# Optimization experiments

Measured on AMD Instinct MI355X. Metric: run time of the kernel, lower is better.

The kernel has to match this reference:

```python
import jax, jax.numpy as jnp
import numpy as np


def setup_inputs() -> dict:
    key = jax.random.key(0)
    k1, k2, k3 = jax.random.split(key, 3)
    B, S, D, N = 2, 2048, 1024, 16
    H = D // N  # head_dim = 64
    x = jax.random.normal(k1, (B, S, D), dtype=jnp.float32)
    W_qkv = jax.random.normal(k2, (N, D, 3 * H), dtype=jnp.float32) / np.sqrt(D).astype(np.float32)
    W_out = jax.random.normal(k3, (N, H, D), dtype=jnp.float32) / np.sqrt(D).astype(np.float32)
    return {"x": x, "W_qkv": W_qkv, "W_out": W_out}


def reference(x, W_qkv, W_out):
    B, S, D = x.shape
    head_dim = W_qkv.shape[-1] // 3
    # QKV projection per head: [B, N, S, 3*H]
    qkv = jnp.einsum('bsd,ndh->bnsh', x, W_qkv)
    q, k, v = jnp.split(qkv, 3, axis=-1)  # each [B, N, S, H]
    scale = jnp.asarray(1.0 / np.sqrt(head_dim), dtype=x.dtype)
    attn = jnp.einsum('bnqh,bnkh->bnqk', q, k) * scale  # [B, N, S, S]
    # causal mask: -1e10 above the diagonal (matches buffer in original)
    mask = jnp.asarray(-1e10, dtype=x.dtype) * (1.0 - jnp.tril(jnp.ones((S, S), dtype=x.dtype)))
    attn = jax.nn.softmax(attn + mask, axis=-1)
    out = jnp.einsum('bnqk,bnkh->bnqh', attn, v)  # [B, N, S, H]
    # faithful to original: raw row-major reshape [B,N,S,H] -> [B, N*H, S]
    out = out.reshape(B, -1, S)
    # faithful to original einsum: d kept, n and h summed over W_out
    return jnp.einsum('bds,nhd->bsd', out, W_out)
```

## Files before the change

kernel.cpp:

```cpp
#include <hip/hip_runtime.h>
#include <hip/hip_bf16.h>

#define B_ 2
#define S_ 2048
#define D_ 1024
#define N_ 16
#define H_ 64

typedef unsigned short u16;
typedef unsigned int u32;
typedef __bf16 bf16x8 __attribute__((ext_vector_type(8)));
typedef u16 u16x8 __attribute__((ext_vector_type(8)));
typedef u32 u32x2 __attribute__((ext_vector_type(2)));
typedef float f4v __attribute__((ext_vector_type(4)));

__device__ __forceinline__ u16 f2b(float f) {
    u32 u = __builtin_bit_cast(u32, f);
    u32 r = (u + 0x7FFFu + ((u >> 16) & 1u)) >> 16;
    return (u16)r;
}
__device__ __forceinline__ bf16x8 asbf(u16x8 v) { return __builtin_bit_cast(bf16x8, v); }
__device__ __forceinline__ u32 cvtpk(float a, float b) {
    u32 r;
    asm("v_cvt_pk_bf16_f32 %0, %1, %2" : "=v"(r) : "v"(a), "v"(b));
    return r;
}

__global__ __launch_bounds__(256) void k_cvt_x(const float* __restrict__ x,
                                               u16* __restrict__ xb) {
    size_t i = ((size_t)blockIdx.x * 256 + threadIdx.x) * 8;
    float4 f0 = *(const float4*)(x + i);
    float4 f1 = *(const float4*)(x + i + 4);
    u16x8 o;
    o[0] = f2b(f0.x); o[1] = f2b(f0.y); o[2] = f2b(f0.z); o[3] = f2b(f0.w);
    o[4] = f2b(f1.x); o[5] = f2b(f1.y); o[6] = f2b(f1.z); o[7] = f2b(f1.w);
    *(u16x8*)(xb + i) = o;
}

__global__ __launch_bounds__(256) void k_cvt_w(const float* __restrict__ w,
                                               u16* __restrict__ wt) {
    __shared__ float T[64][65];
    const int d0 = blockIdx.x * 64, jt = blockIdx.y, n = blockIdx.z;
    const int j0 = jt * 64;
    const float sc = (jt == 0) ? 0.125f : 1.0f;
    const int t = threadIdx.x;
#pragma unroll
    for (int rep = 0; rep < 4; ++rep) {
        int v = t + rep * 256;
        int row = v >> 4, c4 = v & 15;
        float4 f = *(const float4*)(w + ((size_t)(n * 1024 + d0 + row)) * 192 + j0 + c4 * 4);
        T[row][c4 * 4 + 0] = f.x * sc;
        T[row][c4 * 4 + 1] = f.y * sc;
        T[row][c4 * 4 + 2] = f.z * sc;
        T[row][c4 * 4 + 3] = f.w * sc;
    }
    __syncthreads();
#pragma unroll
    for (int rep = 0; rep < 2; ++rep) {
        int c = t + rep * 256;
        int j = c >> 3, db = c & 7;
        u16x8 o;
#pragma unroll
        for (int e = 0; e < 8; ++e) o[e] = f2b(T[db * 8 + e][j]);
        *(u16x8*)(wt + ((size_t)(n * 192 + j0 + j)) * 1024 + d0 + db * 8) = o;
    }
}

__global__ __launch_bounds__(256) void k_wsum(const float* __restrict__ Wout,
                                              float* __restrict__ wsum) {
    __shared__ float red[16][17];
    const int dd = threadIdx.x & 15, rr = threadIdx.x >> 4;
    const int d = blockIdx.x * 16 + dd;
    float s = 0.f;
    for (int r = rr * 64; r < rr * 64 + 64; ++r) s += Wout[(size_t)r * 1024 + d];
    red[rr][dd] = s;
    __syncthreads();
    if (rr == 0) {
        float t = 0.f;
#pragma unroll
        for (int k = 0; k < 16; ++k) t += red[k][dd];
        wsum[d] = t;
    }
}

__global__ __launch_bounds__(512) void k_qkv(const u16* __restrict__ xb,
                                             const u16* __restrict__ wt,
                                             u16* __restrict__ qbuf,
                                             u16* __restrict__ kbuf,
                                             u16* __restrict__ vt) {
    __shared__ u16 As[128 * 64];
    __shared__ u16 Bst[192 * 64];
    const int st = blockIdx.x, n = blockIdx.y;
    const int t = threadIdx.x;
    const int w = t >> 6, lane = t & 63, hi2 = lane >> 4, lo4 = lane & 15;

    const int arow = t >> 2, aq4 = t & 3, ar7 = arow & 7;
    const u16* Ag = xb + (size_t)(st * 128 + arow) * 1024 + aq4 * 16;
    u16* Al0 = As + arow * 64 + ((aq4 * 16 + 0) ^ (ar7 << 3));
    u16* Al1 = As + arow * 64 + ((aq4 * 16 + 8) ^ (ar7 << 3));
    const int br0 = t >> 3, boff = t & 7;
    const u16* Bg0 = wt + (size_t)(n * 192 + br0) * 1024 + boff * 8;
    const u16* Bg1 = Bg0 + (size_t)64 * 1024;
    const u16* Bg2 = Bg0 + (size_t)128 * 1024;
    const int bsw = (boff * 8) ^ ((br0 & 7) << 3);
    u16* Bl0 = Bst + (br0 + 0) * 64 + bsw;
    u16* Bl1 = Bst + (br0 + 64) * 64 + bsw;
    u16* Bl2 = Bst + (br0 + 128) * 64 + bsw;

    f4v acc[12];
#pragma unroll
    for (int i = 0; i < 12; ++i) acc[i] = (f4v){0.f, 0.f, 0.f, 0.f};

    const int rsw = (lo4 & 7) << 3;
    u16x8 ra0 = *(const u16x8*)(Ag);
    u16x8 ra1 = *(const u16x8*)(Ag + 8);
    u16x8 rb0 = *(const u16x8*)(Bg0);
    u16x8 rb1 = *(const u16x8*)(Bg1);
    u16x8 rb2 = *(const u16x8*)(Bg2);

    for (int kk = 0; kk < 16; ++kk) {
        __syncthreads();
        *(u16x8*)Al0 = ra0;
        *(u16x8*)Al1 = ra1;
        *(u16x8*)Bl0 = rb0;
        *(u16x8*)Bl1 = rb1;
        *(u16x8*)Bl2 = rb2;
        if (kk < 15) {
            int o = (kk + 1) * 64;
            ra0 = *(const u16x8*)(Ag + o);
            ra1 = *(const u16x8*)(Ag + o + 8);
            rb0 = *(const u16x8*)(Bg0 + o);
            rb1 = *(const u16x8*)(Bg1 + o);
            rb2 = *(const u16x8*)(Bg2 + o);
        }
        __syncthreads();
        const u16* ar = As + (w * 16 + lo4) * 64;
        bf16x8 fa0 = asbf(*(const u16x8*)(ar + ((hi2 * 8) ^ rsw)));
        bf16x8 fa1 = asbf(*(const u16x8*)(ar + ((hi2 * 8 + 32) ^ rsw)));
        __builtin_amdgcn_s_setprio(1);
#pragma unroll
        for (int fj = 0; fj < 12; ++fj) {
            const u16* br = Bst + (fj * 16 + lo4) * 64;
            bf16x8 fb0 = asbf(*(const u16x8*)(br + ((hi2 * 8) ^ rsw)));
            bf16x8 fb1 = asbf(*(const u16x8*)(br + ((hi2 * 8 + 32) ^ rsw)));
            acc[fj] = __builtin_amdgcn_mfma_f32_16x16x32_bf16(fa0, fb0, acc[fj], 0, 0, 0);
            acc[fj] = __builtin_amdgcn_mfma_f32_16x16x32_bf16(fa1, fb1, acc[fj], 0, 0, 0);
        }
        __builtin_amdgcn_s_setprio(0);
    }

    const int b = st >> 4, s128 = (st & 15) * 128;
    u16* Cs = As;
#pragma unroll
    for (int sec = 0; sec < 3; ++sec) {
        __syncthreads();
#pragma unroll
        for (int q4 = 0; q4 < 4; ++q4)
#pragma unroll
            for (int r = 0; r < 4; ++r)
                Cs[(w * 16 + hi2 * 4 + r) * 64 + q4 * 16 + lo4] = f2b(acc[sec * 4 + q4][r]);
        __syncthreads();
        if (sec == 2) {
            const int h = t & 63, sb = t >> 6;
            u16x8 o0, o1;
#pragma unroll
            for (int e = 0; e < 8; ++e) o0[e] = Cs[(sb * 16 + e) * 64 + h];
#pragma unroll
            for (int e = 0; e < 8; ++e) o1[e] = Cs[(sb * 16 + 8 + e) * 64 + h];
            u16* dst = vt + ((size_t)(b * 16 + n) * 64 + h) * 2048 + s128 + sb * 16;
            *(u16x8*)dst = o0;
            *(u16x8*)(dst + 8) = o1;
        } else {
            const int row = t >> 2, off = (t & 3) * 16;
            u16* dst = (sec == 0) ? qbuf : kbuf;
            dst += ((size_t)(b * 16 + n) * 2048 + s128 + row) * 64 + off;
            *(u16x8*)dst = *(const u16x8*)(Cs + row * 64 + off);
            *(u16x8*)(dst + 8) = *(const u16x8*)(Cs + row * 64 + off + 8);
        }
    }
}

__global__ __launch_bounds__(512) void k_attn(const u16* __restrict__ qbuf,
                                              const u16* __restrict__ kbuf,
                                              const u16* __restrict__ vt,
                                              float* __restrict__ obuf) {
    __shared__ u16 Ks[64 * 64];
    __shared__ u16 Vs[64 * 64];
    __shared__ u16 Ps[8 * 16 * 64];
    const int p = blockIdx.x;
    const int j = p >> 3;
    const int bn = (p & 7) * 4 + (j & 3);
    const int qb = 15 - (j >> 2);
    const int t = threadIdx.x;
    const int w = t >> 6, lane = t & 63, hi2 = lane >> 4, lo4 = lane & 15;

    const int q = qb * 128 + w * 16 + lo4;
    const u16* Qp = qbuf + ((size_t)bn * 2048 + q) * 64;
    bf16x8 bq0 = asbf(*(const u16x8*)(Qp + hi2 * 8));
    bf16x8 bq1 = asbf(*(const u16x8*)(Qp + 32 + hi2 * 8));

    const int srow = t >> 3, so = t & 7;
    const u16* Kg = kbuf + (size_t)bn * 2048 * 64 + (size_t)srow * 64 + so * 8;
    const u16* Vg = vt + (size_t)bn * 64 * 2048 + (size_t)srow * 2048 + so * 8;
    u16* Kl = Ks + srow * 64 + ((so * 8) ^ ((srow & 7) << 3));
    u16* Vl = Vs + srow * 64 + ((so * 8) ^ ((srow & 7) << 3));

    f4v accO[4];
#pragma unroll
    for (int i = 0; i < 4; ++i) accO[i] = (f4v){0.f, 0.f, 0.f, 0.f};
    float m = -3.0e38f, l = 0.f;

    const int rsw = (lo4 & 7) << 3;
    u16* Pw = Ps + w * 1024 + lo4 * 64;
    const int nkb = 2 * qb + 2;

    u16x8 kreg = *(const u16x8*)(Kg);
    u16x8 vreg = *(const u16x8*)(Vg);

    for (int kb = 0; kb < nkb; ++kb) {
        __syncthreads();
        *(u16x8*)Kl = kreg;
        *(u16x8*)Vl = vreg;
        if (kb + 1 < nkb) {
            kreg = *(const u16x8*)(Kg + (size_t)(kb + 1) * 4096);
            vreg = *(const u16x8*)(Vg + (kb + 1) * 64);
        }
        __syncthreads();

        f4v s4[4];
#pragma unroll
        for (int i = 0; i < 4; ++i) s4[i] = (f4v){0.f, 0.f, 0.f, 0.f};
        __builtin_amdgcn_s_setprio(1);
#pragma unroll
        for (int fi = 0; fi < 4; ++fi) {
            const u16* kr = Ks + (fi * 16 + lo4) * 64;
            bf16x8 ka0 = asbf(*(const u16x8*)(kr + ((hi2 * 8) ^ rsw)));
            bf16x8 ka1 = asbf(*(const u16x8*)(kr + ((hi2 * 8 + 32) ^ rsw)));
            s4[fi] = __builtin_amdgcn_mfma_f32_16x16x32_bf16(ka0, bq0, s4[fi], 0, 0, 0);
            s4[fi] = __builtin_amdgcn_mfma_f32_16x16x32_bf16(ka1, bq1, s4[fi], 0, 0, 0);
        }
        __builtin_amdgcn_s_setprio(0);

        if (kb >= 2 * qb) {
#pragma unroll
            for (int fi = 0; fi < 4; ++fi)
#pragma unroll
                for (int r = 0; r < 4; ++r) {
                    int kvg = kb * 64 + fi * 16 + hi2 * 4 + r;
                    if (kvg > q) s4[fi][r] = -3.0e38f;
                }
        }

        float pm = s4[0][0];
#pragma unroll
        for (int fi = 0; fi < 4; ++fi)
#pragma unroll
            for (int r = 0; r < 4; ++r) pm = fmaxf(pm, s4[fi][r]);
        pm = fmaxf(pm, __shfl_xor(pm, 16));
        pm = fmaxf(pm, __shfl_xor(pm, 32));
        float mn = fmaxf(m, pm);
        float fs = __expf(m - mn);
        m = mn;
        float ts = 0.f;
#pragma unroll
        for (int fi = 0; fi < 4; ++fi) {
#pragma unroll
            for (int r = 0; r < 4; ++r) {
                float pv = __expf(s4[fi][r] - mn);
                s4[fi][r] = pv;
                ts += pv;
            }
            u32x2 pk;
            pk[0] = cvtpk(s4[fi][0], s4[fi][1]);
            pk[1] = cvtpk(s4[fi][2], s4[fi][3]);
            *(u32x2*)(Pw + ((fi * 16 + hi2 * 4) ^ rsw)) = pk;
        }
        ts += __shfl_xor(ts, 16);
        ts += __shfl_xor(ts, 32);
        l = l * fs + ts;
#pragma unroll
        for (int fh = 0; fh < 4; ++fh)
#pragma unroll
            for (int r = 0; r < 4; ++r) accO[fh][r] *= fs;

        bf16x8 pb0 = asbf(*(const u16x8*)(Pw + ((hi2 * 8) ^ rsw)));
        bf16x8 pb1 = asbf(*(const u16x8*)(Pw + ((32 + hi2 * 8) ^ rsw)));
        __builtin_amdgcn_s_setprio(1);
#pragma unroll
        for (int fh = 0; fh < 4; ++fh) {
            const u16* vr = Vs + (fh * 16 + lo4) * 64;
            bf16x8 va0 = asbf(*(const u16x8*)(vr + ((hi2 * 8) ^ rsw)));
            bf16x8 va1 = asbf(*(const u16x8*)(vr + ((hi2 * 8 + 32) ^ rsw)));
            accO[fh] = __builtin_amdgcn_mfma_f32_16x16x32_bf16(va0, pb0, accO[fh], 0, 0, 0);
            accO[fh] = __builtin_amdgcn_mfma_f32_16x16x32_bf16(va1, pb1, accO[fh], 0, 0, 0);
        }
        __builtin_amdgcn_s_setprio(0);
    }

    float inv = 1.f / l;
    float* orow = obuf + ((size_t)bn * 2048 + q) * 64;
#pragma unroll
    for (int fh = 0; fh < 4; ++fh)
#pragma unroll
        for (int r = 0; r < 4; ++r)
            orow[fh * 16 + hi2 * 4 + r] = accO[fh][r] * inv;
}

__global__ __launch_bounds__(256) void k_perm(const float* __restrict__ obuf,
                                              const float* __restrict__ wsum,
                                              float* __restrict__ out) {
    __shared__ float T[64][65];
    const int tt = blockIdx.x, n = blockIdx.y, b = blockIdx.z;
    const int tid = threadIdx.x;
    const float* src = obuf + ((size_t)(b * 16 + n) * S_) * H_;
#pragma unroll
    for (int rep = 0; rep < 4; ++rep) {
        int v = tid + rep * 256;
        int r = v >> 4, h4 = v & 15;
        float4 f = *(const float4*)(src + (size_t)(r * 32 + tt) * H_ + h4 * 4);
        T[r][h4 * 4 + 0] = f.x;
        T[r][h4 * 4 + 1] = f.y;
        T[r][h4 * 4 + 2] = f.z;
        T[r][h4 * 4 + 3] = f.w;
    }
    __syncthreads();
#pragma unroll
    for (int rep = 0; rep < 4; ++rep) {
        int v = tid + rep * 256;
        int h = v >> 4, r4 = v & 15;
        float4 w4 = *(const float4*)(wsum + n * 64 + r4 * 4);
        float4 o4 = make_float4(T[r4 * 4 + 0][h] * w4.x, T[r4 * 4 + 1][h] * w4.y,
                                T[r4 * 4 + 2][h] * w4.z, T[r4 * 4 + 3][h] * w4.w);
        *(float4*)(out + ((size_t)(b * S_ + tt * 64 + h) * D_) + n * 64 + r4 * 4) = o4;
    }
}

extern "C" void kernel_launch(void* const* d_in, const int* in_sizes, int n_in,
                              void* d_out, int out_size, void* d_ws, size_t ws_size,
                              hipStream_t stream) {
    const float* x = (const float*)d_in[0];
    const float* Wqkv = (const float*)d_in[1];
    const float* Wout = (const float*)d_in[2];
    float* out = (float*)d_out;

    char* p = (char*)d_ws;
    float* wsum = (float*)p; p += 4096;
    u16* xb = (u16*)p; p += (size_t)4096 * 1024 * 2;
    u16* wt = (u16*)p; p += (size_t)16 * 192 * 1024 * 2;
    u16* qb_ = (u16*)p; p += (size_t)32 * 2048 * 64 * 2;
    u16* kb_ = (u16*)p; p += (size_t)32 * 2048 * 64 * 2;
    u16* vt_ = (u16*)p; p += (size_t)32 * 2048 * 64 * 2;
    float* ob_ = (float*)p;

    k_cvt_x<<<2048, 256, 0, stream>>>(x, xb);
    k_cvt_w<<<dim3(16, 3, 16), 256, 0, stream>>>(Wqkv, wt);
    k_wsum<<<64, 256, 0, stream>>>(Wout, wsum);
    k_qkv<<<dim3(32, 16), 512, 0, stream>>>(xb, wt, qb_, kb_, vt_);
    k_attn<<<512, 512, 0, stream>>>(qb_, kb_, vt_, ob_);
    k_perm<<<dim3(32, 16, 2), 256, 0, stream>>>(ob_, wsum, out);
}
```

Before: 101.0 us.

## Retile QKV GEMM per warp, use 128-wide KV blocks, lazy exp2 rescaling

```diff
diff --git a/kernel.cpp b/kernel.cpp
--- a/kernel.cpp
+++ b/kernel.cpp
@@ -42,7 +42,7 @@
     __shared__ float T[64][65];
     const int d0 = blockIdx.x * 64, jt = blockIdx.y, n = blockIdx.z;
     const int j0 = jt * 64;
-    const float sc = (jt == 0) ? 0.125f : 1.0f;
+    const float sc = (jt == 0) ? 0.125f * 1.44269504089f : 1.0f;
     const int t = threadIdx.x;
 #pragma unroll
     for (int rep = 0; rep < 4; ++rep) {
@@ -93,23 +93,27 @@
     const int st = blockIdx.x, n = blockIdx.y;
     const int t = threadIdx.x;
     const int w = t >> 6, lane = t & 63, hi2 = lane >> 4, lo4 = lane & 15;
-
-    const int arow = t >> 2, aq4 = t & 3, ar7 = arow & 7;
+    const int wm = w >> 2, wn = w & 3;
+
+    const int arow = t >> 2, aq4 = t & 3;
     const u16* Ag = xb + (size_t)(st * 128 + arow) * 1024 + aq4 * 16;
-    u16* Al0 = As + arow * 64 + ((aq4 * 16 + 0) ^ (ar7 << 3));
-    u16* Al1 = As + arow * 64 + ((aq4 * 16 + 8) ^ (ar7 << 3));
-    const int br0 = t >> 3, boff = t & 7;
-    const u16* Bg0 = wt + (size_t)(n * 192 + br0) * 1024 + boff * 8;
+    const int asw = (arow & 7) << 3;
+    u16* Al0 = As + arow * 64 + ((aq4 * 16 + 0) ^ asw);
+    u16* Al1 = As + arow * 64 + ((aq4 * 16 + 8) ^ asw);
+    const int bj = t >> 3, boff = (t & 7) * 8;
+    const u16* Bg0 = wt + (size_t)(n * 192 + bj) * 1024 + boff;
     const u16* Bg1 = Bg0 + (size_t)64 * 1024;
     const u16* Bg2 = Bg0 + (size_t)128 * 1024;
-    const int bsw = (boff * 8) ^ ((br0 & 7) << 3);
-    u16* Bl0 = Bst + (br0 + 0) * 64 + bsw;
-    u16* Bl1 = Bst + (br0 + 64) * 64 + bsw;
-    u16* Bl2 = Bst + (br0 + 128) * 64 + bsw;
-
-    f4v acc[12];
-#pragma unroll
-    for (int i = 0; i < 12; ++i) acc[i] = (f4v){0.f, 0.f, 0.f, 0.f};
+    const int bsw = boff ^ ((bj & 7) << 3);
+    u16* Bl0 = Bst + (bj + 0) * 64 + bsw;
+    u16* Bl1 = Bst + (bj + 64) * 64 + bsw;
+    u16* Bl2 = Bst + (bj + 128) * 64 + bsw;
+
+    f4v acc[4][3];
+#pragma unroll
+    for (int i = 0; i < 4; ++i)
+#pragma unroll
+        for (int j = 0; j < 3; ++j) acc[i][j] = (f4v){0.f, 0.f, 0.f, 0.f};
 
     const int rsw = (lo4 & 7) << 3;
     u16x8 ra0 = *(const u16x8*)(Ag);
@@ -134,17 +138,24 @@
             rb2 = *(const u16x8*)(Bg2 + o);
         }
         __syncthreads();
-        const u16* ar = As + (w * 16 + lo4) * 64;
-        bf16x8 fa0 = asbf(*(const u16x8*)(ar + ((hi2 * 8) ^ rsw)));
-        bf16x8 fa1 = asbf(*(const u16x8*)(ar + ((hi2 * 8 + 32) ^ rsw)));
+        bf16x8 fa[4][2];
+#pragma unroll
+        for (int ms = 0; ms < 4; ++ms) {
+            const u16* ar = As + (wm * 64 + ms * 16 + lo4) * 64;
+            fa[ms][0] = asbf(*(const u16x8*)(ar + ((hi2 * 8) ^ rsw)));
+            fa[ms][1] = asbf(*(const u16x8*)(ar + ((hi2 * 8 + 32) ^ rsw)));
+        }
         __builtin_amdgcn_s_setprio(1);
 #pragma unroll
-        for (int fj = 0; fj < 12; ++fj) {
-            const u16* br = Bst + (fj * 16 + lo4) * 64;
+        for (int fj = 0; fj < 3; ++fj) {
+            const u16* br = Bst + (wn * 48 + fj * 16 + lo4) * 64;
             bf16x8 fb0 = asbf(*(const u16x8*)(br + ((hi2 * 8) ^ rsw)));
             bf16x8 fb1 = asbf(*(const u16x8*)(br + ((hi2 * 8 + 32) ^ rsw)));
-            acc[fj] = __builtin_amdgcn_mfma_f32_16x16x32_bf16(fa0, fb0, acc[fj], 0, 0, 0);
-            acc[fj] = __builtin_amdgcn_mfma_f32_16x16x32_bf16(fa1, fb1, acc[fj], 0, 0, 0);
+#pragma unroll
+            for (int ms = 0; ms < 4; ++ms) {
+                acc[ms][fj] = __builtin_amdgcn_mfma_f32_16x16x32_bf16(fa[ms][0], fb0, acc[ms][fj], 0, 0, 0);
+                acc[ms][fj] = __builtin_amdgcn_mfma_f32_16x16x32_bf16(fa[ms][1], fb1, acc[ms][fj], 0, 0, 0);
+            }
         }
         __builtin_amdgcn_s_setprio(0);
     }
@@ -155,10 +166,17 @@
     for (int sec = 0; sec < 3; ++sec) {
         __syncthreads();
 #pragma unroll
-        for (int q4 = 0; q4 < 4; ++q4)
-#pragma unroll
-            for (int r = 0; r < 4; ++r)
-                Cs[(w * 16 + hi2 * 4 + r) * 64 + q4 * 16 + lo4] = f2b(acc[sec * 4 + q4][r]);
+        for (int fj = 0; fj < 3; ++fj) {
+            const int base = wn * 48 + fj * 16;
+            if ((base >> 6) == sec) {
+                const int col = base - sec * 64 + lo4;
+#pragma unroll
+                for (int ms = 0; ms < 4; ++ms)
+#pragma unroll
+                    for (int r = 0; r < 4; ++r)
+                        Cs[(wm * 64 + ms * 16 + hi2 * 4 + r) * 64 + col] = f2b(acc[ms][fj][r]);
+            }
+        }
         __syncthreads();
         if (sec == 2) {
             const int h = t & 63, sb = t >> 6;
@@ -184,9 +202,9 @@
                                               const u16* __restrict__ kbuf,
                                               const u16* __restrict__ vt,
                                               float* __restrict__ obuf) {
-    __shared__ u16 Ks[64 * 64];
-    __shared__ u16 Vs[64 * 64];
-    __shared__ u16 Ps[8 * 16 * 64];
+    __shared__ u16 Ks[128 * 64];
+    __shared__ u16 Vs[64 * 128];
+    __shared__ u16 Ps[8 * 16 * 128];
     const int p = blockIdx.x;
     const int j = p >> 3;
     const int bn = (p & 7) * 4 + (j & 3);
@@ -199,11 +217,16 @@
     bf16x8 bq0 = asbf(*(const u16x8*)(Qp + hi2 * 8));
     bf16x8 bq1 = asbf(*(const u16x8*)(Qp + 32 + hi2 * 8));
 
-    const int srow = t >> 3, so = t & 7;
-    const u16* Kg = kbuf + (size_t)bn * 2048 * 64 + (size_t)srow * 64 + so * 8;
-    const u16* Vg = vt + (size_t)bn * 64 * 2048 + (size_t)srow * 2048 + so * 8;
-    u16* Kl = Ks + srow * 64 + ((so * 8) ^ ((srow & 7) << 3));
-    u16* Vl = Vs + srow * 64 + ((so * 8) ^ ((srow & 7) << 3));
+    const int krow = t >> 2, kq4 = t & 3;
+    const u16* Kg = kbuf + (size_t)bn * 2048 * 64 + (size_t)krow * 64 + kq4 * 16;
+    const int ksw = (krow & 7) << 3;
+    u16* Kl0 = Ks + krow * 64 + ((kq4 * 16 + 0) ^ ksw);
+    u16* Kl1 = Ks + krow * 64 + ((kq4 * 16 + 8) ^ ksw);
+    const int vrow = t >> 3, vo = (t & 7) * 16;
+    const u16* Vg = vt + (size_t)bn * 64 * 2048 + (size_t)vrow * 2048 + vo;
+    const int vsw = (vrow & 7) << 3;
+    u16* Vl0 = Vs + vrow * 128 + ((vo + 0) ^ vsw);
+    u16* Vl1 = Vs + vrow * 128 + ((vo + 8) ^ vsw);
 
     f4v accO[4];
 #pragma unroll
@@ -211,28 +234,34 @@
     float m = -3.0e38f, l = 0.f;
 
     const int rsw = (lo4 & 7) << 3;
-    u16* Pw = Ps + w * 1024 + lo4 * 64;
-    const int nkb = 2 * qb + 2;
-
-    u16x8 kreg = *(const u16x8*)(Kg);
-    u16x8 vreg = *(const u16x8*)(Vg);
+    u16* Pw = Ps + w * 2048 + lo4 * 128;
+    const int nkb = qb + 1;
+
+    u16x8 kr0 = *(const u16x8*)(Kg);
+    u16x8 kr1 = *(const u16x8*)(Kg + 8);
+    u16x8 vr0 = *(const u16x8*)(Vg);
+    u16x8 vr1 = *(const u16x8*)(Vg + 8);
 
     for (int kb = 0; kb < nkb; ++kb) {
         __syncthreads();
-        *(u16x8*)Kl = kreg;
-        *(u16x8*)Vl = vreg;
+        *(u16x8*)Kl0 = kr0;
+        *(u16x8*)Kl1 = kr1;
+        *(u16x8*)Vl0 = vr0;
+        *(u16x8*)Vl1 = vr1;
         if (kb + 1 < nkb) {
-            kreg = *(const u16x8*)(Kg + (size_t)(kb + 1) * 4096);
-            vreg = *(const u16x8*)(Vg + (kb + 1) * 64);
-        }
-        __syncthreads();
-
-        f4v s4[4];
-#pragma unroll
-        for (int i = 0; i < 4; ++i) s4[i] = (f4v){0.f, 0.f, 0.f, 0.f};
+            kr0 = *(const u16x8*)(Kg + (size_t)(kb + 1) * 8192);
+            kr1 = *(const u16x8*)(Kg + (size_t)(kb + 1) * 8192 + 8);
+            vr0 = *(const u16x8*)(Vg + (kb + 1) * 128);
+            vr1 = *(const u16x8*)(Vg + (kb + 1) * 128 + 8);
+        }
+        __syncthreads();
+
+        f4v s4[8];
+#pragma unroll
+        for (int i = 0; i < 8; ++i) s4[i] = (f4v){0.f, 0.f, 0.f, 0.f};
         __builtin_amdgcn_s_setprio(1);
 #pragma unroll
-        for (int fi = 0; fi < 4; ++fi) {
+        for (int fi = 0; fi < 8; ++fi) {
             const u16* kr = Ks + (fi * 16 + lo4) * 64;
             bf16x8 ka0 = asbf(*(const u16x8*)(kr + ((hi2 * 8) ^ rsw)));
             bf16x8 ka1 = asbf(*(const u16x8*)(kr + ((hi2 * 8 + 32) ^ rsw)));
@@ -241,32 +270,40 @@
         }
         __builtin_amdgcn_s_setprio(0);
 
-        if (kb >= 2 * qb) {
-#pragma unroll
-            for (int fi = 0; fi < 4; ++fi)
+        if (kb == qb) {
+#pragma unroll
+            for (int fi = 0; fi < 8; ++fi)
 #pragma unroll
                 for (int r = 0; r < 4; ++r) {
-                    int kvg = kb * 64 + fi * 16 + hi2 * 4 + r;
+                    int kvg = kb * 128 + fi * 16 + hi2 * 4 + r;
                     if (kvg > q) s4[fi][r] = -3.0e38f;
                 }
         }
 
         float pm = s4[0][0];
 #pragma unroll
-        for (int fi = 0; fi < 4; ++fi)
+        for (int fi = 0; fi < 8; ++fi)
 #pragma unroll
             for (int r = 0; r < 4; ++r) pm = fmaxf(pm, s4[fi][r]);
         pm = fmaxf(pm, __shfl_xor(pm, 16));
         pm = fmaxf(pm, __shfl_xor(pm, 32));
-        float mn = fmaxf(m, pm);
-        float fs = __expf(m - mn);
-        m = mn;
+
         float ts = 0.f;
-#pragma unroll
-        for (int fi = 0; fi < 4; ++fi) {
+        if (__any(pm > m + 8.0f)) {
+            float mn = fmaxf(m, pm);
+            float fs = __builtin_exp2f(m - mn);
+            m = mn;
+            l *= fs;
+#pragma unroll
+            for (int fh = 0; fh < 4; ++fh)
+#pragma unroll
+                for (int r = 0; r < 4; ++r) accO[fh][r] *= fs;
+        }
+#pragma unroll
+        for (int fi = 0; fi < 8; ++fi) {
 #pragma unroll
             for (int r = 0; r < 4; ++r) {
-                float pv = __expf(s4[fi][r] - mn);
+                float pv = __builtin_exp2f(s4[fi][r] - m);
                 s4[fi][r] = pv;
                 ts += pv;
             }
@@ -277,22 +314,21 @@
         }
         ts += __shfl_xor(ts, 16);
         ts += __shfl_xor(ts, 32);
-        l = l * fs + ts;
-#pragma unroll
-        for (int fh = 0; fh < 4; ++fh)
-#pragma unroll
-            for (int r = 0; r < 4; ++r) accO[fh][r] *= fs;
-
-        bf16x8 pb0 = asbf(*(const u16x8*)(Pw + ((hi2 * 8) ^ rsw)));
-        bf16x8 pb1 = asbf(*(const u16x8*)(Pw + ((32 + hi2 * 8) ^ rsw)));
+        l += ts;
+
+        bf16x8 pb[4];
+#pragma unroll
+        for (int ks = 0; ks < 4; ++ks)
+            pb[ks] = asbf(*(const u16x8*)(Pw + ((ks * 32 + hi2 * 8) ^ rsw)));
         __builtin_amdgcn_s_setprio(1);
 #pragma unroll
         for (int fh = 0; fh < 4; ++fh) {
-            const u16* vr = Vs + (fh * 16 + lo4) * 64;
-            bf16x8 va0 = asbf(*(const u16x8*)(vr + ((hi2 * 8) ^ rsw)));
-            bf16x8 va1 = asbf(*(const u16x8*)(vr + ((hi2 * 8 + 32) ^ rsw)));
-            accO[fh] = __builtin_amdgcn_mfma_f32_16x16x32_bf16(va0, pb0, accO[fh], 0, 0, 0);
-            accO[fh] = __builtin_amdgcn_mfma_f32_16x16x32_bf16(va1, pb1, accO[fh], 0, 0, 0);
+            const u16* vr = Vs + (fh * 16 + lo4) * 128;
+#pragma unroll
+            for (int ks = 0; ks < 4; ++ks) {
+                bf16x8 va = asbf(*(const u16x8*)(vr + ((ks * 32 + hi2 * 8) ^ rsw)));
+                accO[fh] = __builtin_amdgcn_mfma_f32_16x16x32_bf16(va, pb[ks], accO[fh], 0, 0, 0);
+            }
         }
         __builtin_amdgcn_s_setprio(0);
     }
```

Measured after the change: 107.9 us. 1.07x slower.
